# Performance work log

Hardware: AMD Instinct MI355X
Metric: run time of the kernel (lower is better)

## Reference

```python
import jax, jax.numpy as jnp
import numpy as np
from jax import lax

B, C, H, W = 16, 64, 256, 256
EPS = 1e-5


def conv2d(x, w, b, pad):
    # x: [B,Cin,H,W], w: [Cout,Cin,kh,kw]
    out = lax.conv_general_dilated(x, w, (1, 1), [(pad, pad), (pad, pad)],
                                   dimension_numbers=("NCHW", "OIHW", "NCHW"))
    return out + b[None, :, None, None]


def setup_inputs() -> dict:
    key = jax.random.key(0)
    ks = jax.random.split(key, 12)
    s = 0.05
    return {
        "x": jax.random.normal(ks[0], (B, C, H, W), jnp.float32),
        "conv_w": jax.random.normal(ks[1], (C, C, 3, 3), jnp.float32) * s,
        "conv_b": jax.random.normal(ks[2], (C,), jnp.float32) * s,
        "bn_gamma": jnp.ones((C,), jnp.float32),
        "bn_beta": jnp.zeros((C,), jnp.float32),
        "bn_mean": jax.random.normal(ks[3], (C,), jnp.float32) * s,
        "bn_var": jax.random.uniform(ks[4], (C,), jnp.float32, 0.5, 1.5),
        "attn_w": jax.random.normal(ks[5], (1, C, 1, 1), jnp.float32) * s,
        "attn_b": jax.random.normal(ks[6], (1,), jnp.float32) * s,
        "dir1_w": jax.random.normal(ks[7], (8, C, 1, 1), jnp.float32) * s,
        "dir1_b": jax.random.normal(ks[8], (8,), jnp.float32) * s,
        "dir2_w": jax.random.normal(ks[9], (1, 8, 1, 1), jnp.float32) * s,
        "dir2_b": jax.random.normal(ks[10], (1,), jnp.float32) * s,
    }


def reference(x, conv_w, conv_b, bn_gamma, bn_beta, bn_mean, bn_var,
              attn_w, attn_b, dir1_w, dir1_b, dir2_w, dir2_b):
    # conv -> BN (eval) -> ReLU
    feat = conv2d(x, conv_w, conv_b, pad=1)
    feat = (feat - bn_mean[None, :, None, None]) * (
        bn_gamma[None, :, None, None] * lax.rsqrt(bn_var + EPS)[None, :, None, None]
    ) + bn_beta[None, :, None, None]
    feat = jax.nn.relu(feat)

    # direction branch: global avg pool -> 1x1 conv -> relu -> 1x1 conv -> sigmoid
    pooled = jnp.mean(x, axis=(2, 3))                      # [B,C]
    h1 = jax.nn.relu(pooled @ dir1_w[:, :, 0, 0].T + dir1_b)  # [B,8]
    direction = jax.nn.sigmoid(h1 @ dir2_w[:, :, 0, 0].T + dir2_b)  # [B,1]
    direction = direction[:, :, None, None]                # [B,1,1,1]

    # attention map [B,1,H,W]
    att = jnp.einsum("bchw,oc->bohw", feat, attn_w[:, :, 0, 0]) + attn_b[None, :, None, None]

    # trapezoid mask: per-row weight depending on direction > 0.5
    j = jnp.arange(H, dtype=x.dtype) / H                   # [H]
    w_up = 0.5 + 0.5 * j
    w_dn = 1.0 - 0.5 * j
    cond = direction[:, 0, 0, 0] > 0.5                     # [B]
    mask = jnp.where(cond[:, None], w_up[None, :], w_dn[None, :])  # [B,H]
    mask = mask[:, None, :, None]                          # [B,1,H,1]

    att = jax.nn.sigmoid(att * mask)
    return x * att, direction
```

## Files before the change

### kernel.cpp

```cpp
#include <hip/hip_runtime.h>
#include <hip/hip_bf16.h>

typedef __attribute__((ext_vector_type(8))) short  s8v;
typedef __attribute__((ext_vector_type(4))) float  f4v;
typedef __attribute__((ext_vector_type(4))) unsigned short u4v;

#define XH 256
#define XW 256
#define XC 64
#define PLANE 65536
#define PCW 66

__device__ __forceinline__ unsigned short f2bf(float f){
  __hip_bfloat16 h = __float2bfloat16(f);
  return __builtin_bit_cast(unsigned short, h);
}
__device__ __forceinline__ float bf2f(unsigned short h){
  unsigned int u = ((unsigned int)h) << 16;
  return __builtin_bit_cast(float, u);
}

__global__ __launch_bounds__(256) void pool_k(const float* __restrict__ x,
                                              float* __restrict__ pooled){
  int plane = blockIdx.x, t = threadIdx.x;
  const f4v* p = (const f4v*)(x + (size_t)plane * PLANE);
  float s = 0.f;
  #pragma unroll 8
  for(int it = 0; it < 64; ++it){
    f4v v = p[t + (it << 8)];
    s += v[0] + v[1] + v[2] + v[3];
  }
  #pragma unroll
  for(int m = 32; m >= 1; m >>= 1) s += __shfl_xor(s, m);
  __shared__ float ps[4];
  if((t & 63) == 0) ps[t >> 6] = s;
  __syncthreads();
  if(t == 0) pooled[plane] = (ps[0] + ps[1] + ps[2] + ps[3]) * (1.f / 65536.f);
}

__global__ __launch_bounds__(256) void prep_k(const float* __restrict__ convw,
    const float* __restrict__ convb, const float* __restrict__ gamma,
    const float* __restrict__ beta,  const float* __restrict__ mean,
    const float* __restrict__ var,   const float* __restrict__ d1w,
    const float* __restrict__ d1b,   const float* __restrict__ d2w,
    const float* __restrict__ d2b,   const float* __restrict__ pooled,
    float* __restrict__ dirv, float* __restrict__ bias2,
    unsigned short* __restrict__ pk, float* __restrict__ outdir){
  int blk = blockIdx.x, t = threadIdx.x;
  if(blk == 0){
    __shared__ float h1s[16][8];
    if(t < 128){
      int b = t >> 3, o = t & 7;
      float a = d1b[o];
      #pragma unroll 8
      for(int c = 0; c < 64; ++c) a = fmaf(pooled[b * 64 + c], d1w[o * 64 + c], a);
      h1s[b][o] = fmaxf(a, 0.f);
    } else if(t >= 128 && t < 192){
      int oc = t - 128;
      float sc = gamma[oc] * rsqrtf(var[oc] + 1e-5f);
      bias2[oc] = (convb[oc] - mean[oc]) * sc + beta[oc];
    }
    __syncthreads();
    if(t < 16){
      float logit = d2b[0];
      #pragma unroll
      for(int o = 0; o < 8; ++o) logit = fmaf(h1s[t][o], d2w[o], logit);
      float dv = 1.f / (1.f + __expf(-logit));
      dirv[t] = dv;
      outdir[t] = dv;
    }
  } else {
    int idx = ((blk - 1) << 8) + t;
    int j = idx & 7, g = (idx >> 3) & 3, n = (idx >> 5) & 63, s = idx >> 11;
    int c = ((s & 1) << 5) + (g << 3) + j, tap = s >> 1;
    float sc = gamma[n] * rsqrtf(var[n] + 1e-5f);
    pk[idx] = f2bf(convw[(n * 64 + c) * 9 + tap] * sc);
  }
}

__global__ __launch_bounds__(256, 3) void main_k(const float* __restrict__ x,
    const float* __restrict__ attnw, const float* __restrict__ attnb,
    const float* __restrict__ dirv,  const float* __restrict__ bias2,
    const unsigned short* __restrict__ pk, float* __restrict__ out){
  __shared__ __align__(16) char lds[6 * PCW * 128 + 4 * 64 * 4];
  float* att_s = (float*)(lds + 6 * PCW * 128);

  const int bid = blockIdx.x;
  const int bs  = ((bid & 7) << 9) | (bid >> 3);
  const int wblk = bs & 3, hblk = (bs >> 2) & 63, b = bs >> 8;
  const int w0 = wblk << 6, h0 = hblk << 2;
  const int t = threadIdx.x, lane = t & 63, wv = t >> 6;
  const int lm = lane & 15, lg = lane >> 4;
  const size_t bbase = (size_t)b * XC * PLANE;

  const char* pkl = (const char*)pk + lm * 64 + (lg << 4);

#define BLOAD(BUF, S) { \
    _Pragma("unroll") \
    for(int jn = 0; jn < 4; ++jn) BUF[jn] = *(const s8v*)(pkl + ((S) << 12) + (jn << 10)); }

  s8v bb0[4], bb1[4], bb2[4];
  BLOAD(bb0, 0); BLOAD(bb1, 1); BLOAD(bb2, 2);

  #pragma unroll 1
  for(int it = 0; it < 7; ++it){
    int task = t + (it << 8);
    if(task < 1728){
      int cgrp = task & 15;
      unsigned rem = (unsigned)task >> 4;
      int hh = rem % 6u;  int chunk = rem / 6u;
      int hhg = h0 - 1 + hh;
      int wcg = w0 - 4 + (chunk << 2);
      f4v v0 = {0,0,0,0}, v1 = {0,0,0,0}, v2 = {0,0,0,0}, v3 = {0,0,0,0};
      if(hhg >= 0 && hhg < XH && wcg >= 0 && wcg + 3 < XW){
        const float* bp = x + bbase + (size_t)(cgrp << 2) * PLANE + (size_t)hhg * XW + wcg;
        v0 = *(const f4v*)bp;
        v1 = *(const f4v*)(bp + PLANE);
        v2 = *(const f4v*)(bp + 2 * PLANE);
        v3 = *(const f4v*)(bp + 3 * PLANE);
      }
      #pragma unroll
      for(int e = 0; e < 4; ++e){
        int pc = (chunk << 2) - 3 + e;
        if(pc >= 0 && pc < PCW){
          int pix = hh * PCW + pc;
          int bo = pix * 128 + ((cgrp << 3) ^ ((pix & 7) << 4));
          u4v pv; pv[0] = f2bf(v0[e]); pv[1] = f2bf(v1[e]);
                  pv[2] = f2bf(v2[e]); pv[3] = f2bf(v3[e]);
          *(u4v*)(lds + bo) = pv;
        }
      }
    }
  }
  __syncthreads();

  f4v acc[4][4];
  #pragma unroll
  for(int i = 0; i < 4; ++i)
    #pragma unroll
    for(int j = 0; j < 4; ++j) acc[i][j] = (f4v){0.f, 0.f, 0.f, 0.f};

  const int pixb = (wv + 1) * PCW + lm + 1;
  const int cbg  = lg << 4;

#define ALOAD(AFR, D, CB) { \
    _Pragma("unroll") \
    for(int i = 0; i < 4; ++i){ int pix = pixb + (i << 4) + (D); \
      AFR[i] = *(const s8v*)(lds + pix * 128 + ((CB) ^ ((pix & 7) << 4))); } }
#define MF(AFR, BUF) { \
    _Pragma("unroll") \
    for(int i = 0; i < 4; ++i){ _Pragma("unroll") for(int j = 0; j < 4; ++j) \
      acc[i][j] = __builtin_amdgcn_mfma_f32_16x16x32_bf16(AFR[i], BUF[j], acc[i][j], 0, 0, 0); } }
#define STEPX(S, BUF) { \
    s8v afr[4]; \
    const int dd = (((S) >> 1) / 3 - 1) * PCW + (((S) >> 1) % 3 - 1); \
    ALOAD(afr, dd, (((S) & 1) ? cbg + 64 : cbg)); \
    __builtin_amdgcn_s_setprio(1); \
    MF(afr, BUF); \
    __builtin_amdgcn_s_setprio(0); \
    if((S) + 3 < 18) BLOAD(BUF, (S) + 3); }

  STEPX(0,  bb0) STEPX(1,  bb1) STEPX(2,  bb2)
  STEPX(3,  bb0) STEPX(4,  bb1) STEPX(5,  bb2)
  STEPX(6,  bb0) STEPX(7,  bb1) STEPX(8,  bb2)
  STEPX(9,  bb0) STEPX(10, bb1) STEPX(11, bb2)
  STEPX(12, bb0) STEPX(13, bb1) STEPX(14, bb2)
  STEPX(15, bb0) STEPX(16, bb1) STEPX(17, bb2)

  float aw[4], bz[4];
  #pragma unroll
  for(int j = 0; j < 4; ++j){ aw[j] = attnw[(j << 4) + lm]; bz[j] = bias2[(j << 4) + lm]; }
  #pragma unroll
  for(int i = 0; i < 4; ++i){
    #pragma unroll
    for(int r = 0; r < 4; ++r){
      float lsum = 0.f;
      #pragma unroll
      for(int j = 0; j < 4; ++j)
        lsum = fmaf(aw[j], fmaxf(acc[i][j][r] + bz[j], 0.f), lsum);
      lsum += __shfl_xor(lsum, 8);
      lsum += __shfl_xor(lsum, 4);
      lsum += __shfl_xor(lsum, 2);
      lsum += __shfl_xor(lsum, 1);
      if(lm == (i << 2) + r) att_s[(wv << 6) + (i << 4) + (lg << 2) + r] = lsum;
    }
  }
  __syncthreads();

  const int col = lane, row = wv;
  const float dir = dirv[b];
  const int h = h0 + row;
  const float jf = (float)h * (1.f / 256.f);
  const float maskv = (dir > 0.5f) ? (0.5f + 0.5f * jf) : (1.f - 0.5f * jf);
  const float att = att_s[(row << 6) + col] + attnb[0];
  const float sg = 1.f / (1.f + __expf(-att * maskv));
  const int pix = (row + 1) * PCW + (col + 1);
  const char* xr = lds + pix * 128;
  const int swz = (pix & 7) << 4;
  float* op = out + bbase + (size_t)h * XW + w0 + col;
  #pragma unroll
  for(int k = 0; k < 8; ++k){
    s8v v = *(const s8v*)(xr + ((k << 4) ^ swz));
    #pragma unroll
    for(int e = 0; e < 8; ++e){
      op[(size_t)((k << 3) + e) * PLANE] = bf2f((unsigned short)v[e]) * sg;
    }
  }
#undef ALOAD
#undef BLOAD
#undef MF
#undef STEPX
}

extern "C" void kernel_launch(void* const* d_in, const int* in_sizes, int n_in,
                              void* d_out, int out_size, void* d_ws, size_t ws_size,
                              hipStream_t stream){
  const float* x     = (const float*)d_in[0];
  const float* convw = (const float*)d_in[1];
  const float* convb = (const float*)d_in[2];
  const float* gamma = (const float*)d_in[3];
  const float* beta  = (const float*)d_in[4];
  const float* mean  = (const float*)d_in[5];
  const float* var   = (const float*)d_in[6];
  const float* attnw = (const float*)d_in[7];
  const float* attnb = (const float*)d_in[8];
  const float* d1w   = (const float*)d_in[9];
  const float* d1b   = (const float*)d_in[10];
  const float* d2w   = (const float*)d_in[11];
  const float* d2b   = (const float*)d_in[12];
  float* out = (float*)d_out;
  char*  ws  = (char*)d_ws;
  float* pooled = (float*)ws;
  float* dirv   = (float*)(ws + 4096);
  float* bias2  = (float*)(ws + 4160);
  unsigned short* pk = (unsigned short*)(ws + 4416);
  float* outdir = out + (size_t)16 * 64 * 256 * 256;

  pool_k<<<1024, 256, 0, stream>>>(x, pooled);
  prep_k<<<145, 256, 0, stream>>>(convw, convb, gamma, beta, mean, var,
                                  d1w, d1b, d2w, d2b, pooled, dirv, bias2, pk, outdir);
  main_k<<<4096, 256, 0, stream>>>(x, attnw, attnb, dirv, bias2, pk, out);
}
```

Before: 631.8 us.

## Pre-transpose input to padded bf16 NHWC buffer and read it directly in conv

A new first kernel converts x into a zero-padded bf16 channels-last image in workspace, and computes per-slab partial channel sums so pooling happens in the same pass. The main conv kernel drops its LDS staging and halo-conversion stage and loads MFMA A fragments straight from global memory, with fewer B buffers and a higher occupancy bound. This trades one extra full read/write of a half-size copy of x for cheaper, LDS-free main-kernel loads, and it relies on cache hits for the 3x3 overlapping reads.

```diff
diff --git a/kernel.cpp b/kernel.cpp
--- a/kernel.cpp
+++ b/kernel.cpp
@@ -3,13 +3,13 @@
 
 typedef __attribute__((ext_vector_type(8))) short  s8v;
 typedef __attribute__((ext_vector_type(4))) float  f4v;
-typedef __attribute__((ext_vector_type(4))) unsigned short u4v;
 
 #define XH 256
 #define XW 256
-#define XC 64
 #define PLANE 65536
-#define PCW 66
+#define X16W 258
+#define X16PITCH (X16W * 128)
+#define X16IMG ((size_t)X16PITCH * 258)
 
 __device__ __forceinline__ unsigned short f2bf(float f){
   __hip_bfloat16 h = __float2bfloat16(f);
@@ -20,22 +20,75 @@
   return __builtin_bit_cast(float, u);
 }
 
-__global__ __launch_bounds__(256) void pool_k(const float* __restrict__ x,
-                                              float* __restrict__ pooled){
-  int plane = blockIdx.x, t = threadIdx.x;
-  const f4v* p = (const f4v*)(x + (size_t)plane * PLANE);
-  float s = 0.f;
-  #pragma unroll 8
-  for(int it = 0; it < 64; ++it){
-    f4v v = p[t + (it << 8)];
-    s += v[0] + v[1] + v[2] + v[3];
-  }
-  #pragma unroll
-  for(int m = 32; m >= 1; m >>= 1) s += __shfl_xor(s, m);
-  __shared__ float ps[4];
-  if((t & 63) == 0) ps[t >> 6] = s;
+__global__ __launch_bounds__(256) void tr_k(const float* __restrict__ x,
+    char* __restrict__ x16, float* __restrict__ part){
+  __shared__ __align__(16) char tile[256 * 128];
+  __shared__ float red[16][16][4];
+  const int bid = blockIdx.x, t = threadIdx.x;
+  const int b = bid >> 6, slab = bid & 63;
+  char* xb = x16 + (size_t)b * X16IMG;
+  const float* xsrc = x + (size_t)b * 64 * PLANE;
+  const int lane = t & 63, q = t & 15, wg16 = t >> 4;
+  float psum[4] = {0.f, 0.f, 0.f, 0.f};
+
+  if(t < 128){
+    int side = t >> 6, r = (t >> 4) & 3, qq = t & 15;
+    char* p = xb + (size_t)(slab * 4 + r + 1) * X16PITCH
+                 + (side ? (size_t)257 * 128 : 0) + qq * 8;
+    *(unsigned long long*)p = 0ULL;
+  }
+  if(slab == 0 || slab == 63){
+    char* rp = xb + (slab ? (size_t)257 * X16PITCH : 0);
+    for(int px = wg16; px < 258; px += 16)
+      *(unsigned long long*)(rp + (size_t)px * 128 + q * 8) = 0ULL;
+  }
+
+  for(int r = 0; r < 4; ++r){
+    const int hg = slab * 4 + r;
+    #pragma unroll
+    for(int it = 0; it < 4; ++it){
+      const int cgrp = (t >> 6) + 4 * it;
+      const float* bp = xsrc + (size_t)(cgrp << 2) * PLANE + hg * 256 + (lane << 2);
+      f4v v0 = *(const f4v*)bp;
+      f4v v1 = *(const f4v*)(bp + PLANE);
+      f4v v2 = *(const f4v*)(bp + 2 * PLANE);
+      f4v v3 = *(const f4v*)(bp + 3 * PLANE);
+      const int slot = cgrp ^ (lane & 15);
+      #pragma unroll
+      for(int e = 0; e < 4; ++e){
+        int w = (lane << 2) + e;
+        unsigned long long d =
+            (unsigned long long)f2bf(v0[e])
+          | ((unsigned long long)f2bf(v1[e]) << 16)
+          | ((unsigned long long)f2bf(v2[e]) << 32)
+          | ((unsigned long long)f2bf(v3[e]) << 48);
+        *(unsigned long long*)(tile + w * 128 + (slot << 3)) = d;
+      }
+    }
+    __syncthreads();
+    char* rowp = xb + (size_t)(hg + 1) * X16PITCH + 128;
+    #pragma unroll 4
+    for(int i = 0; i < 16; ++i){
+      int w = i * 16 + wg16;
+      unsigned long long v = *(const unsigned long long*)
+          (tile + w * 128 + (((q ^ ((w >> 2) & 15))) << 3));
+      unsigned short* sp = (unsigned short*)&v;
+      psum[0] += bf2f(sp[0]); psum[1] += bf2f(sp[1]);
+      psum[2] += bf2f(sp[2]); psum[3] += bf2f(sp[3]);
+      *(unsigned long long*)(rowp + (size_t)w * 128 + (q << 3)) = v;
+    }
+    __syncthreads();
+  }
+  red[wg16][q][0] = psum[0]; red[wg16][q][1] = psum[1];
+  red[wg16][q][2] = psum[2]; red[wg16][q][3] = psum[3];
   __syncthreads();
-  if(t == 0) pooled[plane] = (ps[0] + ps[1] + ps[2] + ps[3]) * (1.f / 65536.f);
+  if(t < 64){
+    int qq = t >> 2, j = t & 3;
+    float s = 0.f;
+    #pragma unroll
+    for(int k = 0; k < 16; ++k) s += red[k][qq][j];
+    part[bid * 64 + (qq << 2) + j] = s;
+  }
 }
 
 __global__ __launch_bounds__(256) void prep_k(const float* __restrict__ convw,
@@ -43,17 +96,25 @@
     const float* __restrict__ beta,  const float* __restrict__ mean,
     const float* __restrict__ var,   const float* __restrict__ d1w,
     const float* __restrict__ d1b,   const float* __restrict__ d2w,
-    const float* __restrict__ d2b,   const float* __restrict__ pooled,
+    const float* __restrict__ d2b,   const float* __restrict__ part,
     float* __restrict__ dirv, float* __restrict__ bias2,
     unsigned short* __restrict__ pk, float* __restrict__ outdir){
   int blk = blockIdx.x, t = threadIdx.x;
   if(blk == 0){
+    __shared__ float pooled_s[16][64];
     __shared__ float h1s[16][8];
+    for(int p = t; p < 1024; p += 256){
+      int b = p >> 6, c = p & 63;
+      float s = 0.f;
+      for(int sl = 0; sl < 64; ++sl) s += part[((b << 6) | sl) * 64 + c];
+      pooled_s[b][c] = s * (1.f / 65536.f);
+    }
+    __syncthreads();
     if(t < 128){
       int b = t >> 3, o = t & 7;
       float a = d1b[o];
       #pragma unroll 8
-      for(int c = 0; c < 64; ++c) a = fmaf(pooled[b * 64 + c], d1w[o * 64 + c], a);
+      for(int c = 0; c < 64; ++c) a = fmaf(pooled_s[b][c], d1w[o * 64 + c], a);
       h1s[b][o] = fmaxf(a, 0.f);
     } else if(t >= 128 && t < 192){
       int oc = t - 128;
@@ -78,12 +139,11 @@
   }
 }
 
-__global__ __launch_bounds__(256, 3) void main_k(const float* __restrict__ x,
+__global__ __launch_bounds__(256, 4) void main_k(const char* __restrict__ x16,
     const float* __restrict__ attnw, const float* __restrict__ attnb,
     const float* __restrict__ dirv,  const float* __restrict__ bias2,
     const unsigned short* __restrict__ pk, float* __restrict__ out){
-  __shared__ __align__(16) char lds[6 * PCW * 128 + 4 * 64 * 4];
-  float* att_s = (float*)(lds + 6 * PCW * 128);
+  __shared__ float att_s[256];
 
   const int bid = blockIdx.x;
   const int bs  = ((bid & 7) << 9) | (bid >> 3);
@@ -91,7 +151,7 @@
   const int w0 = wblk << 6, h0 = hblk << 2;
   const int t = threadIdx.x, lane = t & 63, wv = t >> 6;
   const int lm = lane & 15, lg = lane >> 4;
-  const size_t bbase = (size_t)b * XC * PLANE;
+  const char* xb = x16 + (size_t)b * X16IMG;
 
   const char* pkl = (const char*)pk + lm * 64 + (lg << 4);
 
@@ -99,40 +159,12 @@
     _Pragma("unroll") \
     for(int jn = 0; jn < 4; ++jn) BUF[jn] = *(const s8v*)(pkl + ((S) << 12) + (jn << 10)); }
 
-  s8v bb0[4], bb1[4], bb2[4];
-  BLOAD(bb0, 0); BLOAD(bb1, 1); BLOAD(bb2, 2);
-
-  #pragma unroll 1
-  for(int it = 0; it < 7; ++it){
-    int task = t + (it << 8);
-    if(task < 1728){
-      int cgrp = task & 15;
-      unsigned rem = (unsigned)task >> 4;
-      int hh = rem % 6u;  int chunk = rem / 6u;
-      int hhg = h0 - 1 + hh;
-      int wcg = w0 - 4 + (chunk << 2);
-      f4v v0 = {0,0,0,0}, v1 = {0,0,0,0}, v2 = {0,0,0,0}, v3 = {0,0,0,0};
-      if(hhg >= 0 && hhg < XH && wcg >= 0 && wcg + 3 < XW){
-        const float* bp = x + bbase + (size_t)(cgrp << 2) * PLANE + (size_t)hhg * XW + wcg;
-        v0 = *(const f4v*)bp;
-        v1 = *(const f4v*)(bp + PLANE);
-        v2 = *(const f4v*)(bp + 2 * PLANE);
-        v3 = *(const f4v*)(bp + 3 * PLANE);
-      }
-      #pragma unroll
-      for(int e = 0; e < 4; ++e){
-        int pc = (chunk << 2) - 3 + e;
-        if(pc >= 0 && pc < PCW){
-          int pix = hh * PCW + pc;
-          int bo = pix * 128 + ((cgrp << 3) ^ ((pix & 7) << 4));
-          u4v pv; pv[0] = f2bf(v0[e]); pv[1] = f2bf(v1[e]);
-                  pv[2] = f2bf(v2[e]); pv[3] = f2bf(v3[e]);
-          *(u4v*)(lds + bo) = pv;
-        }
-      }
-    }
-  }
-  __syncthreads();
+  s8v bb0[4], bb1[4];
+  BLOAD(bb0, 0); BLOAD(bb1, 1);
+
+  const char* rb0 = xb + (size_t)(h0 + wv)     * X16PITCH + (size_t)(w0 + lm) * 128 + (lg << 4);
+  const char* rb1 = xb + (size_t)(h0 + wv + 1) * X16PITCH + (size_t)(w0 + lm) * 128 + (lg << 4);
+  const char* rb2 = xb + (size_t)(h0 + wv + 2) * X16PITCH + (size_t)(w0 + lm) * 128 + (lg << 4);
 
   f4v acc[4][4];
   #pragma unroll
@@ -140,32 +172,26 @@
     #pragma unroll
     for(int j = 0; j < 4; ++j) acc[i][j] = (f4v){0.f, 0.f, 0.f, 0.f};
 
-  const int pixb = (wv + 1) * PCW + lm + 1;
-  const int cbg  = lg << 4;
-
-#define ALOAD(AFR, D, CB) { \
-    _Pragma("unroll") \
-    for(int i = 0; i < 4; ++i){ int pix = pixb + (i << 4) + (D); \
-      AFR[i] = *(const s8v*)(lds + pix * 128 + ((CB) ^ ((pix & 7) << 4))); } }
 #define MF(AFR, BUF) { \
     _Pragma("unroll") \
     for(int i = 0; i < 4; ++i){ _Pragma("unroll") for(int j = 0; j < 4; ++j) \
       acc[i][j] = __builtin_amdgcn_mfma_f32_16x16x32_bf16(AFR[i], BUF[j], acc[i][j], 0, 0, 0); } }
 #define STEPX(S, BUF) { \
     s8v afr[4]; \
-    const int dd = (((S) >> 1) / 3 - 1) * PCW + (((S) >> 1) % 3 - 1); \
-    ALOAD(afr, dd, (((S) & 1) ? cbg + 64 : cbg)); \
+    const char* rp = ((S) >> 1) / 3 == 0 ? rb0 : (((S) >> 1) / 3 == 1 ? rb1 : rb2); \
+    const int off = (((S) >> 1) % 3) * 128 + (((S) & 1) << 6); \
+    _Pragma("unroll") \
+    for(int i = 0; i < 4; ++i) afr[i] = *(const s8v*)(rp + off + (i << 11)); \
     __builtin_amdgcn_s_setprio(1); \
     MF(afr, BUF); \
     __builtin_amdgcn_s_setprio(0); \
-    if((S) + 3 < 18) BLOAD(BUF, (S) + 3); }
-
-  STEPX(0,  bb0) STEPX(1,  bb1) STEPX(2,  bb2)
-  STEPX(3,  bb0) STEPX(4,  bb1) STEPX(5,  bb2)
-  STEPX(6,  bb0) STEPX(7,  bb1) STEPX(8,  bb2)
-  STEPX(9,  bb0) STEPX(10, bb1) STEPX(11, bb2)
-  STEPX(12, bb0) STEPX(13, bb1) STEPX(14, bb2)
-  STEPX(15, bb0) STEPX(16, bb1) STEPX(17, bb2)
+    if((S) + 2 < 18) BLOAD(BUF, (S) + 2); }
+
+  STEPX(0,  bb0) STEPX(1,  bb1) STEPX(2,  bb0) STEPX(3,  bb1)
+  STEPX(4,  bb0) STEPX(5,  bb1) STEPX(6,  bb0) STEPX(7,  bb1)
+  STEPX(8,  bb0) STEPX(9,  bb1) STEPX(10, bb0) STEPX(11, bb1)
+  STEPX(12, bb0) STEPX(13, bb1) STEPX(14, bb0) STEPX(15, bb1)
+  STEPX(16, bb0) STEPX(17, bb1)
 
   float aw[4], bz[4];
   #pragma unroll
@@ -194,19 +220,16 @@
   const float maskv = (dir > 0.5f) ? (0.5f + 0.5f * jf) : (1.f - 0.5f * jf);
   const float att = att_s[(row << 6) + col] + attnb[0];
   const float sg = 1.f / (1.f + __expf(-att * maskv));
-  const int pix = (row + 1) * PCW + (col + 1);
-  const char* xr = lds + pix * 128;
-  const int swz = (pix & 7) << 4;
-  float* op = out + bbase + (size_t)h * XW + w0 + col;
+  const char* xr = xb + (size_t)(h + 1) * X16PITCH + (size_t)(w0 + col + 1) * 128;
+  float* op = out + (size_t)b * 64 * PLANE + (size_t)h * XW + w0 + col;
   #pragma unroll
   for(int k = 0; k < 8; ++k){
-    s8v v = *(const s8v*)(xr + ((k << 4) ^ swz));
+    s8v v = *(const s8v*)(xr + (k << 4));
     #pragma unroll
     for(int e = 0; e < 8; ++e){
       op[(size_t)((k << 3) + e) * PLANE] = bf2f((unsigned short)v[e]) * sg;
     }
   }
-#undef ALOAD
 #undef BLOAD
 #undef MF
 #undef STEPX
@@ -230,14 +253,15 @@
   const float* d2b   = (const float*)d_in[12];
   float* out = (float*)d_out;
   char*  ws  = (char*)d_ws;
-  float* pooled = (float*)ws;
-  float* dirv   = (float*)(ws + 4096);
-  float* bias2  = (float*)(ws + 4160);
-  unsigned short* pk = (unsigned short*)(ws + 4416);
+  float* dirv   = (float*)ws;
+  float* bias2  = (float*)(ws + 256);
+  unsigned short* pk = (unsigned short*)(ws + 1024);
+  float* part   = (float*)(ws + 74752);
+  char*  x16    = ws + 336896;
   float* outdir = out + (size_t)16 * 64 * 256 * 256;
 
-  pool_k<<<1024, 256, 0, stream>>>(x, pooled);
+  tr_k<<<1024, 256, 0, stream>>>(x, x16, part);
   prep_k<<<145, 256, 0, stream>>>(convw, convb, gamma, beta, mean, var,
-                                  d1w, d1b, d2w, d2b, pooled, dirv, bias2, pk, outdir);
-  main_k<<<4096, 256, 0, stream>>>(x, attnw, attnb, dirv, bias2, pk, out);
-}
+                                  d1w, d1b, d2w, d2b, part, dirv, bias2, pk, outdir);
+  main_k<<<4096, 256, 0, stream>>>(x16, attnw, attnb, dirv, bias2, pk, out);
+}
```

After: 782.8 us. 1.24x slower.
